# Performance work log

Hardware: AMD Instinct MI355X
Metric: run time of the kernel (lower is better)

The kernel has to match this reference:

```python
import jax, jax.numpy as jnp
import numpy as np

DIM = 1024
N_OBJ = 2048
N_REL = 4096
H_CAT = 4
H_OUT = 6
OUT_CAT = DIM // 2            # 512, concat=True branch
OUT_NC = (DIM // 2) * H_OUT   # 3072, concat=False branch


def setup_inputs() -> dict:
    key = jax.random.key(0)
    ks = jax.random.split(key, 6)
    s = 0.02
    return {
        "feat_obj": jax.random.normal(ks[0], (N_OBJ, DIM), jnp.float32),
        "feat_rel": jax.random.normal(ks[1], (N_REL, DIM), jnp.float32),
        # 3 concat=True attentions, each with 4 Linears(dim -> dim/2)
        "W_cat": jax.random.normal(ks[2], (3, 4, DIM, OUT_CAT), jnp.float32) * s,
        "b_cat": jax.random.normal(ks[3], (3, 4, OUT_CAT), jnp.float32) * s,
        # 2 used concat=False attentions, each with 4 Linears(dim -> 6*dim/2)
        "W_out": jax.random.normal(ks[4], (2, 4, DIM, OUT_NC), jnp.float32) * s,
        "b_out": jax.random.normal(ks[5], (2, 4, OUT_NC), jnp.float32) * s,
    }


def _mha(xq, xk, Ws, bs, h, mask=None, concat=True):
    # Ws: [4, dim, out_dim], bs: [4, out_dim]
    out_dim = Ws.shape[-1]
    d_k = out_dim // h

    def proj(x, W, b):
        return (x @ W + b).reshape(-1, h, d_k).transpose(1, 0, 2)  # [h, N, d_k]

    q = proj(xq, Ws[0], bs[0])
    k = proj(xk, Ws[1], bs[1])
    qv = proj(xq, Ws[2], bs[2])
    kv = proj(xk, Ws[3], bs[3])
    scores = jnp.einsum('hnd,hmd->hnm', q, k) / jnp.sqrt(jnp.asarray(d_k, q.dtype))
    if mask is not None:
        scores = jnp.where(mask == 0, jnp.asarray(-1e9, scores.dtype), scores)
    p = jax.nn.softmax(scores, axis=-1)          # [h, Nq, Nk]
    a1 = jax.nn.elu(jnp.einsum('hnm,hmd->hnd', p, kv))  # per-head value mix (rows)
    a2 = jax.nn.elu(jnp.einsum('hnm,hnd->hmd', p, qv))  # transposed mix (cols)
    if concat:
        nq, nk = xq.shape[0], xk.shape[0]
        return a1.transpose(1, 0, 2).reshape(nq, out_dim), a2.transpose(1, 0, 2).reshape(nk, out_dim)
    return a1.sum(0), a2.sum(0)


def reference(feat_obj, feat_rel, W_cat, b_cat, W_out, b_out):
    n_obj = feat_obj.shape[0]
    mask = 1.0 - jnp.eye(n_obj, dtype=feat_obj.dtype)  # zero out self-attention

    sub_obj, obj_sub = _mha(feat_obj, feat_obj, W_cat[0], b_cat[0], H_CAT, mask, True)
    sub_rel, rel_sub = _mha(feat_obj, feat_rel, W_cat[1], b_cat[1], H_CAT, None, True)
    rel_obj, obj_rel = _mha(feat_rel, feat_obj, W_cat[2], b_cat[2], H_CAT, None, True)

    obj_feat = (feat_obj
                + jnp.concatenate((sub_obj, obj_sub), axis=1)
                + jnp.concatenate((sub_rel, obj_rel), axis=1)) / 3.0
    rel_feat = (feat_rel + jnp.concatenate((rel_obj, rel_sub), axis=1)) / 2.0

    _, rel_sub2 = _mha(obj_feat, rel_feat, W_out[0], b_out[0], H_OUT, None, False)
    rel_obj2, _ = _mha(rel_feat, obj_feat, W_out[1], b_out[1], H_OUT, None, False)
    rel_feat = (feat_rel + jnp.concatenate((rel_obj2, rel_sub2), axis=1)) / 2.0

    return obj_feat, rel_feat
```

## Files before the change

kernel.cpp:

```cpp
#include <hip/hip_runtime.h>

typedef unsigned short u16;
typedef unsigned int u32;
typedef __attribute__((ext_vector_type(4))) float f32x4;
typedef __attribute__((ext_vector_type(8))) __bf16 bf16x8;
typedef __attribute__((ext_vector_type(8))) unsigned short u16x8;

#if defined(__has_builtin)
#if __has_builtin(__builtin_amdgcn_global_load_lds)
#define HAS_GLL 1
#endif
#endif

__device__ __forceinline__ u16 f2bf(float f) {
    u32 u = __builtin_bit_cast(u32, f);
    u += 0x7fffu + ((u >> 16) & 1u);
    return (u16)(u >> 16);
}
__device__ __forceinline__ float bf2f(u16 x) {
    return __builtin_bit_cast(float, (u32)x << 16);
}

template <int N> __device__ __forceinline__ void wbar() {
#ifdef HAS_GLL
    if constexpr (N == 0)
        asm volatile("s_waitcnt vmcnt(0)\n\ts_barrier" ::: "memory");
    else if constexpr (N == 2)
        asm volatile("s_waitcnt vmcnt(2)\n\ts_barrier" ::: "memory");
    else
        asm volatile("s_waitcnt vmcnt(4)\n\ts_barrier" ::: "memory");
#else
    __syncthreads();
#endif
}

__device__ __forceinline__ void fbar() {
#ifdef HAS_GLL
    asm volatile("s_waitcnt vmcnt(0) lgkmcnt(0)\n\ts_barrier" ::: "memory");
#else
    __syncthreads();
#endif
}

__device__ __forceinline__ void lbar() {
#ifdef HAS_GLL
    asm volatile("s_waitcnt lgkmcnt(0)\n\ts_barrier" ::: "memory");
#else
    __syncthreads();
#endif
}

__global__ __launch_bounds__(256) void zero_kernel(float* __restrict__ p, int n) {
    int i = blockIdx.x * 256 + threadIdx.x;
    if (i < n) p[i] = 0.f;
}

__global__ __launch_bounds__(256) void cvt_bf16_kernel(const float4* __restrict__ in,
                                                       ushort4* __restrict__ out, int n4) {
    int i = blockIdx.x * 256 + threadIdx.x;
    if (i < n4) {
        float4 v = in[i];
        ushort4 o;
        o.x = f2bf(v.x); o.y = f2bf(v.y); o.z = f2bf(v.z); o.w = f2bf(v.w);
        out[i] = o;
    }
}

__global__ __launch_bounds__(256) void transcvt_kernel(const float* __restrict__ W,
                                                       u16* __restrict__ Wt, int K, int N) {
    __shared__ u16 t[32][33];
    int b = blockIdx.z;
    const float* Wb = W + (size_t)b * K * N;
    u16* Wtb = Wt + (size_t)b * K * N;
    int n0 = blockIdx.x * 32, k0 = blockIdx.y * 32;
    int tx = threadIdx.x, ty = threadIdx.y;
#pragma unroll
    for (int j = 0; j < 4; ++j)
        t[ty + j * 8][tx] = f2bf(Wb[(size_t)(k0 + ty + j * 8) * N + n0 + tx]);
    __syncthreads();
#pragma unroll
    for (int j = 0; j < 4; ++j)
        Wtb[(size_t)(n0 + ty + j * 8) * K + k0 + tx] = t[tx][ty + j * 8];
}

__global__ __launch_bounds__(256) void scale_rows_kernel(const u16* __restrict__ in,
                                                         u16* __restrict__ out,
                                                         const float* __restrict__ rd,
                                                         int C, int lgdk, int mul) {
    int i = (blockIdx.x * 256 + threadIdx.x) * 8;
    int r = i / C, c = i % C;
    const float* rdp = rd + ((size_t)(r >> lgdk)) * C + c;
    u16x8 x = *reinterpret_cast<const u16x8*>(in + i);
    u16x8 o;
#pragma unroll
    for (int j = 0; j < 8; ++j)
        o[j] = f2bf(mul ? bf2f(x[j]) * rdp[j] : bf2f(x[j]) / rdp[j]);
    *reinterpret_cast<u16x8*>(out + i) = o;
}

struct FGrp { const u16* A; const u16* B; const u16* V; float* O; float* rs; int M; int NK; int mask; };
struct FCfg { FGrp g[3]; };

template <int NORM>
__global__ __launch_bounds__(256) void fused_attn1_kernel(FCfg cfg, float scale) {
    __shared__ __align__(16) u16 Bbuf[2][4 * 2048];
    __shared__ __align__(16) u16 Vbuf[2][2 * 4096];
    __shared__ __align__(16) u16 Pbuf[2 * 2048];
    __shared__ float rsum_lds[64][2];
    const int gi = blockIdx.z >> 2, h = blockIdx.z & 3;
    FGrp G = (gi == 0) ? cfg.g[0] : (gi == 1) ? cfg.g[1] : cfg.g[2];
    const int row0 = blockIdx.x * 64;
    if (row0 >= G.M) return;
    const u16* Ap = G.A + h * 128;
    const u16* Bp = G.B + h * 128;
    const u16* Vp = G.V + (size_t)h * 128 * G.NK;
    float* Op = G.O + h * 128;
    const int ldv = G.NK;
    const int tid = threadIdx.x, lane = tid & 63, wid = tid >> 6;
    const int swr = (wid >> 1) * 32, swc = (wid & 1) * 32;
    const int pwr = swr, pwc = (wid & 1) * 64;

    auto gld = [&](const u16* src, u16* dst) {
#ifdef HAS_GLL
        __builtin_amdgcn_global_load_lds(
            (const __attribute__((address_space(1))) void*)src,
            (__attribute__((address_space(3))) void*)dst, 16, 0, 0);
#else
        *reinterpret_cast<uint4*>(dst) = *reinterpret_cast<const uint4*>(src);
#endif
    };
    auto stageB = [&](int t, int buf) {
#pragma unroll
        for (int it = 0; it < 4; ++it) {
            int c = tid + it * 256;
            int kb = c >> 8, cc = c & 255;
            int r = cc >> 2, lch = (cc & 3) ^ ((r >> 1) & 3);
            gld(Bp + (size_t)(t * 64 + r) * 512 + kb * 32 + lch * 8, &Bbuf[buf][kb * 2048 + cc * 8]);
        }
    };
    auto stageV = [&](int t, int buf) {
#pragma unroll
        for (int it = 0; it < 4; ++it) {
            int c = tid + it * 256;
            int kb = c >> 9, cc = c & 511;
            int r = cc >> 2, lch = (cc & 3) ^ ((r >> 1) & 3);
            gld(Vp + (size_t)r * ldv + t * 64 + kb * 32 + lch * 8, &Vbuf[buf][kb * 4096 + cc * 8]);
        }
    };

    bf16x8 areg[2][4];
#pragma unroll
    for (int m = 0; m < 2; ++m) {
        int rr = swr + m * 16 + (lane & 15);
#pragma unroll
        for (int kk = 0; kk < 4; ++kk)
            areg[m][kk] = *reinterpret_cast<const bf16x8*>(
                Ap + (size_t)(row0 + rr) * 512 + kk * 32 + (lane >> 4) * 8);
    }
    stageB(0, 0);
    stageV(0, 0);
    stageB(1, 1);
    stageV(1, 1);
    fbar();

    f32x4 accp[2][4] = {};
    float rsum[2][4] = {};
    const int nt = G.NK >> 6;
    for (int t = 0; t < nt; ++t) {
        const int cur = t & 1;
        f32x4 accs[2][2] = {};
#pragma unroll
        for (int kk = 0; kk < 4; ++kk) {
            bf16x8 bf[2];
#pragma unroll
            for (int n = 0; n < 2; ++n) {
                int rr = swc + n * 16 + (lane & 15);
                int p = (lane >> 4) ^ ((rr >> 1) & 3);
                bf[n] = *reinterpret_cast<const bf16x8*>(&Bbuf[cur][kk * 2048 + rr * 32 + p * 8]);
            }
#pragma unroll
            for (int m = 0; m < 2; ++m)
#pragma unroll
                for (int n = 0; n < 2; ++n)
                    accs[m][n] = __builtin_amdgcn_mfma_f32_16x16x32_bf16(areg[m][kk], bf[n], accs[m][n], 0, 0, 0);
        }
#pragma unroll
        for (int m = 0; m < 2; ++m) {
#pragma unroll
            for (int n = 0; n < 2; ++n) {
#pragma unroll
                for (int j = 0; j < 4; ++j) {
                    int prow = swr + m * 16 + ((lane >> 4) << 2) + j;
                    int pkey = swc + n * 16 + (lane & 15);
                    float v = __expf(accs[m][n][j] * scale);
                    if (G.mask && (row0 + prow == t * 64 + pkey)) v = 0.f;
                    if (NORM == 1) rsum[m][j] += v;
                    Pbuf[(pkey >> 5) * 2048 + prow * 32 +
                         ((((pkey >> 3) & 3) ^ ((prow >> 1) & 3)) << 3) + (pkey & 7)] = f2bf(v);
                }
            }
        }
        lbar();
        if (t + 2 < nt) stageB(t + 2, cur);
#pragma unroll
        for (int kk = 0; kk < 2; ++kk) {
            bf16x8 pf[2], vf[4];
#pragma unroll
            for (int m = 0; m < 2; ++m) {
                int rr = pwr + m * 16 + (lane & 15);
                int p = (lane >> 4) ^ ((rr >> 1) & 3);
                pf[m] = *reinterpret_cast<const bf16x8*>(&Pbuf[kk * 2048 + rr * 32 + p * 8]);
            }
#pragma unroll
            for (int n = 0; n < 4; ++n) {
                int dd = pwc + n * 16 + (lane & 15);
                int p = (lane >> 4) ^ ((dd >> 1) & 3);
                vf[n] = *reinterpret_cast<const bf16x8*>(&Vbuf[cur][kk * 4096 + dd * 32 + p * 8]);
            }
#pragma unroll
            for (int m = 0; m < 2; ++m)
#pragma unroll
                for (int n = 0; n < 4; ++n)
                    accp[m][n] = __builtin_amdgcn_mfma_f32_16x16x32_bf16(pf[m], vf[n], accp[m][n], 0, 0, 0);
        }
        if (t + 2 < nt)      wbar<4>();
        else if (t + 1 < nt) wbar<0>();
        if (t + 2 < nt) stageV(t + 2, cur);
    }

    if (NORM == 1) {
#pragma unroll
        for (int m = 0; m < 2; ++m)
#pragma unroll
            for (int j = 0; j < 4; ++j) {
                float s = rsum[m][j];
                s += __shfl_xor(s, 1); s += __shfl_xor(s, 2);
                s += __shfl_xor(s, 4); s += __shfl_xor(s, 8);
                rsum[m][j] = s;
            }
        if ((lane & 15) == 0) {
#pragma unroll
            for (int m = 0; m < 2; ++m)
#pragma unroll
                for (int j = 0; j < 4; ++j)
                    rsum_lds[swr + m * 16 + ((lane >> 4) << 2) + j][wid & 1] = rsum[m][j];
        }
        __syncthreads();
        if (tid < 64)
            G.rs[(size_t)h * G.M + row0 + tid] = 1.f / (rsum_lds[tid][0] + rsum_lds[tid][1]);
#pragma unroll
        for (int m = 0; m < 2; ++m) {
#pragma unroll
            for (int j = 0; j < 4; ++j) {
                int row = pwr + m * 16 + ((lane >> 4) << 2) + j;
                float rd = 1.f / (rsum_lds[row][0] + rsum_lds[row][1]);
#pragma unroll
                for (int n = 0; n < 4; ++n) {
                    float v = accp[m][n][j] * rd;
                    v = v > 0.f ? v : (__expf(v) - 1.f);
                    Op[(size_t)(row0 + row) * 512 + pwc + n * 16 + (lane & 15)] = v;
                }
            }
        }
    } else {
#pragma unroll
        for (int m = 0; m < 2; ++m) {
#pragma unroll
            for (int j = 0; j < 4; ++j) {
                int row = pwr + m * 16 + ((lane >> 4) << 2) + j;
#pragma unroll
                for (int n = 0; n < 4; ++n) {
                    float v = accp[m][n][j];
                    v = v > 0.f ? v : (__expf(v) - 1.f);
                    Op[(size_t)(row0 + row) * 512 + pwc + n * 16 + (lane & 15)] = v;
                }
            }
        }
    }
}

enum { E_PROJ = 0, E_PROJT, E_EXP, E_EXPC, E_EXPT, E_EXPMT, E_PART };

template <int EPI, int BM>
__global__ __launch_bounds__(256) void gemm_nt(const u16* __restrict__ A, const u16* __restrict__ B,
                                               void* __restrict__ Cv, void* __restrict__ CvT,
                                               const float* __restrict__ bias, float* __restrict__ rs,
                                               int M, int N, int K, int lda, int ldb, int ldc, int ldcT,
                                               float scale, long sAz, long sBz, long sCz, long sCzT,
                                               long sBias, long sRs, int ZK, long sAz2, long sBz2) {
    constexpr bool HAS_BIAS = (EPI == E_PROJ || EPI == E_PROJT);
    constexpr bool DO_EXP = (EPI == E_EXP || EPI == E_EXPC || EPI == E_EXPT || EPI == E_EXPMT);
    constexpr bool DO_MASK = (EPI == E_EXPMT);
    constexpr int RSUM = (EPI == E_EXPC) ? 2 : (DO_EXP ? 1 : 0);
    constexpr bool STORE_N = (EPI != E_PROJT);
    constexpr bool STORE_T = (EPI == E_PROJT || EPI == E_EXPT || EPI == E_EXPMT);

    constexpr int MF = BM / 32;
    constexpr int ITERS = BM * 32 / (256 * 8);
    constexpr int LOADS = ITERS * 2;
    constexpr int SM_STAGE = 3 * BM * 64;
    constexpr int SM_REPACK = BM * BM;
    __shared__ __align__(16) u16 smem[SM_STAGE > SM_REPACK ? SM_STAGE : SM_REPACK];
    const int tid = threadIdx.x;
    const int lane = tid & 63;
    const int wid = tid >> 6;
    const int wr = (wid >> 1) * (BM / 2);
    const int wc = (wid & 1) * (BM / 2);
    const int row0 = blockIdx.x * BM;
    const int col0 = blockIdx.y * BM;
    const long zo = blockIdx.z;
    const long hz = zo / ZK;
    const long kz = zo - hz * ZK;
    const u16* Az = A + hz * sAz + kz * sAz2;
    const u16* Bz = B + hz * sBz + kz * sBz2;
    const float* biasz = bias ? bias + zo * sBias : nullptr;
    float* rsz = rs ? rs + zo * sRs : nullptr;
    f32x4 acc[MF][MF] = {};

    auto As = [&](int buf) { return smem + buf * (BM * 64); };
    auto Bs = [&](int buf) { return smem + buf * (BM * 64) + BM * 32; };

    auto stage = [&](int buf, int k0) {
#pragma unroll
        for (int i = 0; i < ITERS; ++i) {
            int c = tid + i * 256;
            int r = c >> 2;
            int lch = (c & 3) ^ ((r >> 1) & 3);
            const u16* sa = Az + (size_t)(row0 + r) * lda + k0 + lch * 8;
            const u16* sb = Bz + (size_t)(col0 + r) * ldb + k0 + lch * 8;
#ifdef HAS_GLL
            __builtin_amdgcn_global_load_lds(
                (const __attribute__((address_space(1))) void*)sa,
                (__attribute__((address_space(3))) void*)(&As(buf)[c * 8]), 16, 0, 0);
            __builtin_amdgcn_global_load_lds(
                (const __attribute__((address_space(1))) void*)sb,
                (__attribute__((address_space(3))) void*)(&Bs(buf)[c * 8]), 16, 0, 0);
#else
            *reinterpret_cast<uint4*>(&As(buf)[c * 8]) = *reinterpret_cast<const uint4*>(sa);
            *reinterpret_cast<uint4*>(&Bs(buf)[c * 8]) = *reinterpret_cast<const uint4*>(sb);
#endif
        }
    };

    stage(0, 0);
    stage(1, 32);
    wbar<LOADS>();

    const int nsteps = K >> 5;
    for (int t = 0; t < nsteps; ++t) {
        const int bufc = t % 3;
        const bool more2 = (t + 2 < nsteps);
        if (more2) stage((t + 2) % 3, (t + 2) << 5);
        bf16x8 af[MF], bv[MF];
#pragma unroll
        for (int m = 0; m < MF; ++m) {
            int rr = wr + m * 16 + (lane & 15);
            int p = (lane >> 4) ^ ((rr >> 1) & 3);
            af[m] = *reinterpret_cast<const bf16x8*>(&As(bufc)[rr * 32 + p * 8]);
        }
#pragma unroll
        for (int n = 0; n < MF; ++n) {
            int rr = wc + n * 16 + (lane & 15);
            int p = (lane >> 4) ^ ((rr >> 1) & 3);
            bv[n] = *reinterpret_cast<const bf16x8*>(&Bs(bufc)[rr * 32 + p * 8]);
        }
#pragma unroll
        for (int m = 0; m < MF; ++m)
#pragma unroll
            for (int n = 0; n < MF; ++n)
                acc[m][n] = __builtin_amdgcn_mfma_f32_16x16x32_bf16(af[m], bv[n], acc[m][n], 0, 0, 0);
        if (more2)                 wbar<LOADS>();
        else if (t + 1 < nsteps)   wbar<0>();
        else                       __syncthreads();
    }

#pragma unroll
    for (int m = 0; m < MF; ++m) {
#pragma unroll
        for (int n = 0; n < MF; ++n) {
#pragma unroll
            for (int j = 0; j < 4; ++j) {
                float v = acc[m][n][j];
                if (HAS_BIAS) v += biasz[col0 + wc + n * 16 + (lane & 15)];
                if (DO_EXP) {
                    v = __expf(v * scale);
                    if (DO_MASK &&
                        row0 + wr + m * 16 + ((lane >> 4) << 2) + j ==
                        col0 + wc + n * 16 + (lane & 15)) v = 0.f;
                }
                acc[m][n][j] = v;
            }
        }
    }

    if (RSUM == 1) {
#pragma unroll
        for (int m = 0; m < MF; ++m) {
#pragma unroll
            for (int j = 0; j < 4; ++j) {
                float p = 0.f;
#pragma unroll
                for (int n = 0; n < MF; ++n) p += acc[m][n][j];
                p += __shfl_xor(p, 1); p += __shfl_xor(p, 2);
                p += __shfl_xor(p, 4); p += __shfl_xor(p, 8);
                if ((lane & 15) == 0)
                    atomicAdd(rsz + row0 + wr + m * 16 + ((lane >> 4) << 2) + j, p);
            }
        }
    } else if (RSUM == 2) {
#pragma unroll
        for (int n = 0; n < MF; ++n) {
            float p = 0.f;
#pragma unroll
            for (int m = 0; m < MF; ++m)
#pragma unroll
                for (int j = 0; j < 4; ++j) p += acc[m][n][j];
            p += __shfl_xor(p, 16); p += __shfl_xor(p, 32);
            if (lane < 16) atomicAdd(rsz + col0 + wc + n * 16 + lane, p);
        }
    }

    char* lc = reinterpret_cast<char*>(smem);
    if (STORE_N) {
#pragma unroll
        for (int m = 0; m < MF; ++m) {
#pragma unroll
            for (int n = 0; n < MF; ++n) {
#pragma unroll
                for (int j = 0; j < 4; ++j) {
                    int lrow = wr + m * 16 + ((lane >> 4) << 2) + j;
                    int lcol = wc + n * 16 + (lane & 15);
                    u32 byte = (u32)((lrow * BM + lcol) * 2) ^ (((lrow >> 2) & 3) << 5);
                    *reinterpret_cast<u16*>(lc + byte) = f2bf(acc[m][n][j]);
                }
            }
        }
        __syncthreads();
        constexpr int CH = BM / 8;
        constexpr int NIT = BM * CH / 256;
        u16* Cp = reinterpret_cast<u16*>(Cv) + zo * sCz;
#pragma unroll
        for (int it = 0; it < NIT; ++it) {
            int idx = it * 256 + tid;
            int rrow = idx / CH, c8 = idx % CH;
            u32 byte = (u32)((rrow * BM + c8 * 8) * 2) ^ (((rrow >> 2) & 3) << 5);
            u16x8 val = *reinterpret_cast<const u16x8*>(lc + byte);
            *reinterpret_cast<u16x8*>(Cp + (size_t)(row0 + rrow) * ldc + col0 + c8 * 8) = val;
        }
    }
    if (STORE_T) {
        __syncthreads();
#pragma unroll
        for (int m = 0; m < MF; ++m) {
#pragma unroll
            for (int n = 0; n < MF; ++n) {
                int lcol = wc + n * 16 + (lane & 15);
                int lrow0 = wr + m * 16 + ((lane >> 4) << 2);
                u32 byte = (u32)((lcol * BM + lrow0) * 2) ^ ((u32)(lcol & 7) << 4);
                u32 lo = (u32)f2bf(acc[m][n][0]) | ((u32)f2bf(acc[m][n][1]) << 16);
                u32 hi = (u32)f2bf(acc[m][n][2]) | ((u32)f2bf(acc[m][n][3]) << 16);
                uint2 pk; pk.x = lo; pk.y = hi;
                *reinterpret_cast<uint2*>(lc + byte) = pk;
            }
        }
        __syncthreads();
        constexpr int CHT = BM / 8;
        constexpr int NITT = BM * CHT / 256;
        u16* Tp = reinterpret_cast<u16*>(CvT) + zo * sCzT;
#pragma unroll
        for (int it = 0; it < NITT; ++it) {
            int idx = it * 256 + tid;
            int c = idx / CHT, r8 = idx % CHT;
            u32 byte = (u32)((c * BM + r8 * 8) * 2) ^ ((u32)(c & 7) << 4);
            u16x8 val = *reinterpret_cast<const u16x8*>(lc + byte);
            *reinterpret_cast<u16x8*>(Tp + (size_t)(col0 + c) * ldcT + row0 + r8 * 8) = val;
        }
    }
}

__global__ __launch_bounds__(256) void reduce_h_elu_kernel(const u16* __restrict__ part,
                                                           float* __restrict__ out, int R, int H,
                                                           const float* __restrict__ rd) {
    int i = blockIdx.x * 256 + threadIdx.x;
    int row = i >> 6, c8 = i & 63;
    long plane = (long)R * 512;
    const u16* p = part + (size_t)row * 512 + c8 * 8;
    float s[8] = {};
    for (int h = 0; h < H; ++h) {
        u16x8 x = *reinterpret_cast<const u16x8*>(p + (size_t)h * plane);
        float r = rd ? 1.f / rd[(size_t)h * R + row] : 1.f;
#pragma unroll
        for (int j = 0; j < 8; ++j) {
            float v = bf2f(x[j]) * r;
            s[j] += v > 0.f ? v : (__expf(v) - 1.f);
        }
    }
    float4* o = reinterpret_cast<float4*>(out + (size_t)row * 512 + c8 * 8);
    o[0] = float4{s[0], s[1], s[2], s[3]};
    o[1] = float4{s[4], s[5], s[6], s[7]};
}

__global__ __launch_bounds__(256) void combine_obj_kernel(const float4* __restrict__ feat,
        const float4* __restrict__ a, const float4* __restrict__ b,
        const float4* __restrict__ c, const float4* __restrict__ d,
        float4* __restrict__ out, ushort4* __restrict__ outbf) {
    int i = blockIdx.x * 256 + threadIdx.x;
    int r = i >> 8, c4 = i & 255;
    size_t half = (size_t)r * 128 + (c4 & 127);
    float4 t1 = (c4 < 128) ? a[half] : b[half];
    float4 t2 = (c4 < 128) ? c[half] : d[half];
    float4 f = feat[i];
    float4 o;
    o.x = (f.x + t1.x + t2.x) * (1.f / 3.f);
    o.y = (f.y + t1.y + t2.y) * (1.f / 3.f);
    o.z = (f.z + t1.z + t2.z) * (1.f / 3.f);
    o.w = (f.w + t1.w + t2.w) * (1.f / 3.f);
    out[i] = o;
    ushort4 ob; ob.x = f2bf(o.x); ob.y = f2bf(o.y); ob.z = f2bf(o.z); ob.w = f2bf(o.w);
    outbf[i] = ob;
}

__global__ __launch_bounds__(256) void combine_rel1_kernel(const float4* __restrict__ feat,
        const float4* __restrict__ a, const float4* __restrict__ b, ushort4* __restrict__ outbf) {
    int i = blockIdx.x * 256 + threadIdx.x;
    int r = i >> 8, c4 = i & 255;
    size_t half = (size_t)r * 128 + (c4 & 127);
    float4 t = (c4 < 128) ? a[half] : b[half];
    float4 f = feat[i];
    ushort4 ob;
    ob.x = f2bf((f.x + t.x) * 0.5f); ob.y = f2bf((f.y + t.y) * 0.5f);
    ob.z = f2bf((f.z + t.z) * 0.5f); ob.w = f2bf((f.w + t.w) * 0.5f);
    outbf[i] = ob;
}

__global__ __launch_bounds__(256) void combine_rel2_kernel(const float4* __restrict__ feat,
        const float4* __restrict__ a, const float4* __restrict__ b, float4* __restrict__ out) {
    int i = blockIdx.x * 256 + threadIdx.x;
    int r = i >> 8, c4 = i & 255;
    size_t half = (size_t)r * 128 + (c4 & 127);
    float4 t = (c4 < 128) ? a[half] : b[half];
    float4 f = feat[i];
    float4 o;
    o.x = (f.x + t.x) * 0.5f; o.y = (f.y + t.y) * 0.5f;
    o.z = (f.z + t.z) * 0.5f; o.w = (f.w + t.w) * 0.5f;
    out[i] = o;
}

extern "C" void kernel_launch(void* const* d_in, const int* in_sizes, int n_in,
                              void* d_out, int out_size, void* d_ws, size_t ws_size,
                              hipStream_t stream) {
    (void)in_sizes; (void)n_in; (void)out_size; (void)ws_size;
    const float* feat_obj = (const float*)d_in[0];
    const float* feat_rel = (const float*)d_in[1];
    const float* W_cat = (const float*)d_in[2];
    const float* b_cat = (const float*)d_in[3];
    const float* W_out = (const float*)d_in[4];
    const float* b_out = (const float*)d_in[5];
    float* out_obj = (float*)d_out;
    float* out_rel = (float*)d_out + (size_t)2048 * 1024;

    char* w = (char*)d_ws;
    auto alloc = [&](size_t bytes) { void* p = (void*)w; w += (bytes + 255) & ~(size_t)255; return p; };
    u16* bf_obj  = (u16*)alloc((size_t)2048 * 1024 * 2);
    u16* bf_rel  = (u16*)alloc((size_t)4096 * 1024 * 2);
    u16* bf_obj2 = (u16*)alloc((size_t)2048 * 1024 * 2);
    u16* bf_rel2 = (u16*)alloc((size_t)4096 * 1024 * 2);
    u16* Wt_cat  = (u16*)alloc((size_t)12 * 512 * 1024 * 2);
    u16* Q01   = (u16*)alloc((size_t)2 * 2048 * 512 * 2);
    u16* K02   = (u16*)alloc((size_t)2 * 2048 * 512 * 2);
    u16* Q2    = (u16*)alloc((size_t)4096 * 512 * 2);
    u16* K1    = (u16*)alloc((size_t)4096 * 512 * 2);
    u16* Vq01T = (u16*)alloc((size_t)2 * 512 * 2048 * 2);
    u16* Vk02T = (u16*)alloc((size_t)2 * 512 * 2048 * 2);
    u16* Vk1T  = (u16*)alloc((size_t)512 * 4096 * 2);
    u16* Vq2T  = (u16*)alloc((size_t)512 * 4096 * 2);
    u16* Pq2   = (u16*)alloc((size_t)2 * 2048 * 3072 * 2);
    u16* Pk2   = (u16*)alloc((size_t)2 * 4096 * 3072 * 2);
    u16* VTa   = (u16*)alloc((size_t)2 * 3072 * 2048 * 2);
    u16* VTs   = (u16*)alloc((size_t)3072 * 2048 * 2);
    u16* Sbuf  = (u16*)alloc((size_t)6 * 4096 * 2048 * 2);
    u16* Wt2   = Sbuf;
    u16* part  = (u16*)alloc((size_t)6 * 4096 * 512 * 2);
    float* rdAll = (float*)alloc((size_t)36864 * 4);
    float* rdQ = rdAll;
    float* rdM = rdAll + 12288;
    float* rs0 = (float*)alloc((size_t)4 * 2048 * 4);
    float* rs1 = (float*)alloc((size_t)4 * 2048 * 4);
    float* rs2 = (float*)alloc((size_t)4 * 4096 * 4);
    float* sub_obj  = (float*)alloc((size_t)2048 * 512 * 4);
    float* obj_sub  = (float*)alloc((size_t)2048 * 512 * 4);
    float* sub_rel  = (float*)alloc((size_t)2048 * 512 * 4);
    float* obj_rel  = (float*)alloc((size_t)2048 * 512 * 4);
    float* rel_obj  = (float*)alloc((size_t)4096 * 512 * 4);
    float* rel_sub  = (float*)alloc((size_t)4096 * 512 * 4);
    float* rel_obj2 = (float*)alloc((size_t)4096 * 512 * 4);
    float* rel_sub2 = (float*)alloc((size_t)4096 * 512 * 4);

    zero_kernel<<<144, 256, 0, stream>>>(rdAll, 36864);
    cvt_bf16_kernel<<<2048, 256, 0, stream>>>((const float4*)feat_obj, (ushort4*)bf_obj, 2048 * 1024 / 4);
    cvt_bf16_kernel<<<4096, 256, 0, stream>>>((const float4*)feat_rel, (ushort4*)bf_rel, 4096 * 1024 / 4);
    transcvt_kernel<<<dim3(16, 32, 12), dim3(32, 8), 0, stream>>>(W_cat, Wt_cat, 1024, 512);
    transcvt_kernel<<<dim3(96, 32, 8), dim3(32, 8), 0, stream>>>(W_out, Wt2, 1024, 3072);

    const float sc1 = 0.08838834764831845f;
    const float sc2 = 0.04419417382415922f;
    const long planeW = (long)512 * 1024;
    const long planeW2 = (long)3072 * 1024;
    const long NIL = 0;

    gemm_nt<E_PROJ, 64><<<dim3(32, 8, 2), 256, 0, stream>>>(
        bf_obj, Wt_cat, Q01, nullptr, b_cat, nullptr,
        2048, 512, 1024, 1024, 1024, 512, 0, 0.f, NIL, 4 * planeW, (long)2048 * 512, NIL,
        4L * 512, NIL, 1, NIL, NIL);
    gemm_nt<E_PROJ, 64><<<dim3(32, 8, 2), 256, 0, stream>>>(
        bf_obj, Wt_cat + planeW, K02, nullptr, b_cat + 512, nullptr,
        2048, 512, 1024, 1024, 1024, 512, 0, 0.f, NIL, 8 * planeW, (long)2048 * 512, NIL,
        8L * 512, NIL, 1, NIL, NIL);
    gemm_nt<E_PROJT, 64><<<dim3(32, 8, 2), 256, 0, stream>>>(
        bf_obj, Wt_cat + 2 * planeW, nullptr, Vq01T, b_cat + 1024, nullptr,
        2048, 512, 1024, 1024, 1024, 0, 2048, 0.f, NIL, 4 * planeW, NIL, (long)512 * 2048,
        4L * 512, NIL, 1, NIL, NIL);
    gemm_nt<E_PROJT, 64><<<dim3(32, 8, 2), 256, 0, stream>>>(
        bf_obj, Wt_cat + 3 * planeW, nullptr, Vk02T, b_cat + 1536, nullptr,
        2048, 512, 1024, 1024, 1024, 0, 2048, 0.f, NIL, 8 * planeW, NIL, (long)512 * 2048,
        8L * 512, NIL, 1, NIL, NIL);
    gemm_nt<E_PROJ, 64><<<dim3(64, 8, 1), 256, 0, stream>>>(
        bf_rel, Wt_cat + 5 * planeW, K1, nullptr, b_cat + 5 * 512, nullptr,
        4096, 512, 1024, 1024, 1024, 512, 0, 0.f, NIL, NIL, NIL, NIL, NIL, NIL, 1, NIL, NIL);
    gemm_nt<E_PROJ, 64><<<dim3(64, 8, 1), 256, 0, stream>>>(
        bf_rel, Wt_cat + 8 * planeW, Q2, nullptr, b_cat + 8 * 512, nullptr,
        4096, 512, 1024, 1024, 1024, 512, 0, 0.f, NIL, NIL, NIL, NIL, NIL, NIL, 1, NIL, NIL);
    gemm_nt<E_PROJT, 64><<<dim3(64, 8, 1), 256, 0, stream>>>(
        bf_rel, Wt_cat + 7 * planeW, nullptr, Vk1T, b_cat + 7 * 512, nullptr,
        4096, 512, 1024, 1024, 1024, 0, 4096, 0.f, NIL, NIL, NIL, NIL, NIL, NIL, 1, NIL, NIL);
    gemm_nt<E_PROJT, 64><<<dim3(64, 8, 1), 256, 0, stream>>>(
        bf_rel, Wt_cat + 10 * planeW, nullptr, Vq2T, b_cat + 10 * 512, nullptr,
        4096, 512, 1024, 1024, 1024, 0, 4096, 0.f, NIL, NIL, NIL, NIL, NIL, NIL, 1, NIL, NIL);

    FCfg f1, f2;
    f1.g[0] = { Q01,                    K02,                    Vk02T,                    sub_obj, rs0, 2048, 2048, 1 };
    f1.g[1] = { Q01 + (size_t)2048*512, K1,                     Vk1T,                     sub_rel, rs1, 2048, 4096, 0 };
    f1.g[2] = { Q2,                     K02 + (size_t)2048*512, Vk02T + (size_t)512*2048, rel_obj, rs2, 4096, 2048, 0 };
    fused_attn1_kernel<1><<<dim3(64, 1, 12), 256, 0, stream>>>(f1, sc1);
    scale_rows_kernel<<<512, 256, 0, stream>>>(Vq01T, Vq01T, rs0, 2048, 7, 1);
    scale_rows_kernel<<<512, 256, 0, stream>>>(Vq01T + (size_t)512 * 2048, Vq01T + (size_t)512 * 2048, rs1, 2048, 7, 1);
    scale_rows_kernel<<<1024, 256, 0, stream>>>(Vq2T, Vq2T, rs2, 4096, 7, 1);
    f2.g[0] = { K02,                    Q01,                    Vq01T,                    obj_sub, rs0, 2048, 2048, 1 };
    f2.g[1] = { K1,                     Q01 + (size_t)2048*512, Vq01T + (size_t)512*2048, rel_sub, rs1, 4096, 2048, 0 };
    f2.g[2] = { K02 + (size_t)2048*512, Q2,                     Vq2T,                     obj_rel, rs2, 2048, 4096, 0 };
    fused_attn1_kernel<0><<<dim3(64, 1, 12), 256, 0, stream>>>(f2, sc1);

    combine_obj_kernel<<<2048, 256, 0, stream>>>((const float4*)feat_obj, (const float4*)sub_obj,
        (const float4*)obj_sub, (const float4*)sub_rel, (const float4*)obj_rel,
        (float4*)out_obj, (ushort4*)bf_obj2);
    combine_rel1_kernel<<<4096, 256, 0, stream>>>((const float4*)feat_rel, (const float4*)rel_obj,
        (const float4*)rel_sub, (ushort4*)bf_rel2);

    gemm_nt<E_PROJ, 128><<<dim3(16, 24, 2), 256, 0, stream>>>(
        bf_obj2, Wt2, Pq2, nullptr, b_out, nullptr,
        2048, 3072, 1024, 1024, 1024, 3072, 0, 0.f, NIL, 5 * planeW2, (long)2048 * 3072, NIL,
        5L * 3072, NIL, 1, NIL, NIL);
    gemm_nt<E_PROJ, 128><<<dim3(32, 24, 2), 256, 0, stream>>>(
        bf_rel2, Wt2 + planeW2, Pk2, nullptr, b_out + 3072, nullptr,
        4096, 3072, 1024, 1024, 1024, 3072, 0, 0.f, NIL, 3 * planeW2, (long)4096 * 3072, NIL,
        3L * 3072, NIL, 1, NIL, NIL);
    gemm_nt<E_PROJT, 128><<<dim3(16, 24, 2), 256, 0, stream>>>(
        bf_obj2, Wt2 + 2 * planeW2, nullptr, VTa, b_out + 2 * 3072, nullptr,
        2048, 3072, 1024, 1024, 1024, 0, 2048, 0.f, NIL, 5 * planeW2, NIL, (long)3072 * 2048,
        5L * 3072, NIL, 1, NIL, NIL);

    const long spl2 = (long)4096 * 2048;
    const long vpl2 = (long)4096 * 512;

    {
        gemm_nt<E_EXPC, 128><<<dim3(32, 16, 6), 256, 0, stream>>>(
            Pk2, Pq2, Sbuf, nullptr, nullptr, rdQ,
            4096, 2048, 512, 3072, 3072, 2048, 0, sc2, 512, 512, spl2, NIL, NIL, 2048, 1, NIL, NIL);
        scale_rows_kernel<<<3072, 256, 0, stream>>>(VTa, VTs, rdQ, 2048, 9, 0);
        gemm_nt<E_PART, 128><<<dim3(32, 4, 6), 256, 0, stream>>>(
            Sbuf, VTs, part, nullptr, nullptr, nullptr,
            4096, 512, 2048, 2048, 2048, 512, 0, 0.f, spl2, 512L * 2048, vpl2, NIL, NIL, NIL,
            1, NIL, NIL);
        reduce_h_elu_kernel<<<1024, 256, 0, stream>>>(part, rel_sub2, 4096, 6, nullptr);
    }
    {
        gemm_nt<E_EXP, 128><<<dim3(32, 16, 6), 256, 0, stream>>>(
            Pk2 + (size_t)4096 * 3072, Pq2 + (size_t)2048 * 3072, Sbuf, nullptr, nullptr, rdM,
            4096, 2048, 512, 3072, 3072, 2048, 0, sc2, 512, 512, spl2, NIL, NIL, 4096, 1, NIL, NIL);
        gemm_nt<E_PART, 128><<<dim3(32, 4, 6), 256, 0, stream>>>(
            Sbuf, VTa + (size_t)3072 * 2048, part, nullptr, nullptr, nullptr,
            4096, 512, 2048, 2048, 2048, 512, 0, 0.f, spl2, 512L * 2048, vpl2, NIL, NIL, NIL,
            1, NIL, NIL);
        reduce_h_elu_kernel<<<1024, 256, 0, stream>>>(part, rel_obj2, 4096, 6, rdM);
    }

    combine_rel2_kernel<<<4096, 256, 0, stream>>>((const float4*)feat_rel, (const float4*)rel_obj2,
        (const float4*)rel_sub2, (float4*)out_rel);
}
```

Measured before the change: 818.1 us.

## Permute concat-branch weights to batch stage-one projections into four GEMM launches

Reorders the twelve concat-branch weight matrices and their biases at conversion time so that projections sharing an input and output layout sit contiguously. The eight stage-one projection GEMMs become four batched launches, and their tile size moves from 64 to 128. Downstream attention groups and scaling kernels are repointed to the new consolidated buffers. This cuts launch overhead and small-grid underutilisation, at the cost of an extra bias permutation kernel and fewer, larger tiles per launch.

New measurement: 792.9 us (median of 2 runs). 1.03x faster.

```diff
diff --git a/kernel.cpp b/kernel.cpp
--- a/kernel.cpp
+++ b/kernel.cpp
@@ -50,6 +50,14 @@
 #endif
 }
 
+__device__ __forceinline__ int s1perm(int b) {
+    switch (b) {
+        case 0: return 0;  case 1: return 2;  case 2: return 4;  case 3: return 6;
+        case 4: return 1;  case 5: return 8;  case 6: return 5;  case 7: return 10;
+        case 8: return 9;  case 9: return 3;  case 10: return 11; default: return 7;
+    }
+}
+
 __global__ __launch_bounds__(256) void zero_kernel(float* __restrict__ p, int n) {
     int i = blockIdx.x * 256 + threadIdx.x;
     if (i < n) p[i] = 0.f;
@@ -81,6 +89,32 @@
 #pragma unroll
     for (int j = 0; j < 4; ++j)
         Wtb[(size_t)(n0 + ty + j * 8) * K + k0 + tx] = t[tx][ty + j * 8];
+}
+
+__global__ __launch_bounds__(256) void transcvt_perm_kernel(const float* __restrict__ W,
+                                                            u16* __restrict__ Wt, int K, int N) {
+    __shared__ u16 t[32][33];
+    int b = blockIdx.z;
+    int d = s1perm(b);
+    const float* Wb = W + (size_t)b * K * N;
+    u16* Wtb = Wt + (size_t)d * K * N;
+    int n0 = blockIdx.x * 32, k0 = blockIdx.y * 32;
+    int tx = threadIdx.x, ty = threadIdx.y;
+#pragma unroll
+    for (int j = 0; j < 4; ++j)
+        t[ty + j * 8][tx] = f2bf(Wb[(size_t)(k0 + ty + j * 8) * N + n0 + tx]);
+    __syncthreads();
+#pragma unroll
+    for (int j = 0; j < 4; ++j)
+        Wtb[(size_t)(n0 + ty + j * 8) * K + k0 + tx] = t[tx][ty + j * 8];
+}
+
+__global__ __launch_bounds__(256) void bias_perm_kernel(const float* __restrict__ in,
+                                                        float* __restrict__ out) {
+    int b = blockIdx.x;
+    int d = s1perm(b);
+    out[d * 512 + threadIdx.x] = in[b * 512 + threadIdx.x];
+    out[d * 512 + 256 + threadIdx.x] = in[b * 512 + 256 + threadIdx.x];
 }
 
 __global__ __launch_bounds__(256) void scale_rows_kernel(const u16* __restrict__ in,
@@ -565,15 +599,12 @@
     u16* bf_rel  = (u16*)alloc((size_t)4096 * 1024 * 2);
     u16* bf_obj2 = (u16*)alloc((size_t)2048 * 1024 * 2);
     u16* bf_rel2 = (u16*)alloc((size_t)4096 * 1024 * 2);
-    u16* Wt_cat  = (u16*)alloc((size_t)12 * 512 * 1024 * 2);
-    u16* Q01   = (u16*)alloc((size_t)2 * 2048 * 512 * 2);
-    u16* K02   = (u16*)alloc((size_t)2 * 2048 * 512 * 2);
-    u16* Q2    = (u16*)alloc((size_t)4096 * 512 * 2);
-    u16* K1    = (u16*)alloc((size_t)4096 * 512 * 2);
-    u16* Vq01T = (u16*)alloc((size_t)2 * 512 * 2048 * 2);
-    u16* Vk02T = (u16*)alloc((size_t)2 * 512 * 2048 * 2);
-    u16* Vk1T  = (u16*)alloc((size_t)512 * 4096 * 2);
-    u16* Vq2T  = (u16*)alloc((size_t)512 * 4096 * 2);
+    u16* WtP     = (u16*)alloc((size_t)12 * 512 * 1024 * 2);
+    float* rbcat = (float*)alloc((size_t)12 * 512 * 4);
+    u16* QKo   = (u16*)alloc((size_t)4 * 2048 * 512 * 2);
+    u16* RelN  = (u16*)alloc((size_t)2 * 4096 * 512 * 2);
+    u16* To    = (u16*)alloc((size_t)4 * 512 * 2048 * 2);
+    u16* RelT  = (u16*)alloc((size_t)2 * 512 * 4096 * 2);
     u16* Pq2   = (u16*)alloc((size_t)2 * 2048 * 3072 * 2);
     u16* Pk2   = (u16*)alloc((size_t)2 * 4096 * 3072 * 2);
     u16* VTa   = (u16*)alloc((size_t)2 * 3072 * 2048 * 2);
@@ -599,7 +630,8 @@
     zero_kernel<<<144, 256, 0, stream>>>(rdAll, 36864);
     cvt_bf16_kernel<<<2048, 256, 0, stream>>>((const float4*)feat_obj, (ushort4*)bf_obj, 2048 * 1024 / 4);
     cvt_bf16_kernel<<<4096, 256, 0, stream>>>((const float4*)feat_rel, (ushort4*)bf_rel, 4096 * 1024 / 4);
-    transcvt_kernel<<<dim3(16, 32, 12), dim3(32, 8), 0, stream>>>(W_cat, Wt_cat, 1024, 512);
+    transcvt_perm_kernel<<<dim3(16, 32, 12), dim3(32, 8), 0, stream>>>(W_cat, WtP, 1024, 512);
+    bias_perm_kernel<<<12, 256, 0, stream>>>(b_cat, rbcat);
     transcvt_kernel<<<dim3(96, 32, 8), dim3(32, 8), 0, stream>>>(W_out, Wt2, 1024, 3072);
 
     const float sc1 = 0.08838834764831845f;
@@ -607,47 +639,35 @@
     const long planeW = (long)512 * 1024;
     const long planeW2 = (long)3072 * 1024;
     const long NIL = 0;
-
-    gemm_nt<E_PROJ, 64><<<dim3(32, 8, 2), 256, 0, stream>>>(
-        bf_obj, Wt_cat, Q01, nullptr, b_cat, nullptr,
-        2048, 512, 1024, 1024, 1024, 512, 0, 0.f, NIL, 4 * planeW, (long)2048 * 512, NIL,
-        4L * 512, NIL, 1, NIL, NIL);
-    gemm_nt<E_PROJ, 64><<<dim3(32, 8, 2), 256, 0, stream>>>(
-        bf_obj, Wt_cat + planeW, K02, nullptr, b_cat + 512, nullptr,
-        2048, 512, 1024, 1024, 1024, 512, 0, 0.f, NIL, 8 * planeW, (long)2048 * 512, NIL,
-        8L * 512, NIL, 1, NIL, NIL);
-    gemm_nt<E_PROJT, 64><<<dim3(32, 8, 2), 256, 0, stream>>>(
-        bf_obj, Wt_cat + 2 * planeW, nullptr, Vq01T, b_cat + 1024, nullptr,
-        2048, 512, 1024, 1024, 1024, 0, 2048, 0.f, NIL, 4 * planeW, NIL, (long)512 * 2048,
-        4L * 512, NIL, 1, NIL, NIL);
-    gemm_nt<E_PROJT, 64><<<dim3(32, 8, 2), 256, 0, stream>>>(
-        bf_obj, Wt_cat + 3 * planeW, nullptr, Vk02T, b_cat + 1536, nullptr,
-        2048, 512, 1024, 1024, 1024, 0, 2048, 0.f, NIL, 8 * planeW, NIL, (long)512 * 2048,
-        8L * 512, NIL, 1, NIL, NIL);
-    gemm_nt<E_PROJ, 64><<<dim3(64, 8, 1), 256, 0, stream>>>(
-        bf_rel, Wt_cat + 5 * planeW, K1, nullptr, b_cat + 5 * 512, nullptr,
-        4096, 512, 1024, 1024, 1024, 512, 0, 0.f, NIL, NIL, NIL, NIL, NIL, NIL, 1, NIL, NIL);
-    gemm_nt<E_PROJ, 64><<<dim3(64, 8, 1), 256, 0, stream>>>(
-        bf_rel, Wt_cat + 8 * planeW, Q2, nullptr, b_cat + 8 * 512, nullptr,
-        4096, 512, 1024, 1024, 1024, 512, 0, 0.f, NIL, NIL, NIL, NIL, NIL, NIL, 1, NIL, NIL);
-    gemm_nt<E_PROJT, 64><<<dim3(64, 8, 1), 256, 0, stream>>>(
-        bf_rel, Wt_cat + 7 * planeW, nullptr, Vk1T, b_cat + 7 * 512, nullptr,
-        4096, 512, 1024, 1024, 1024, 0, 4096, 0.f, NIL, NIL, NIL, NIL, NIL, NIL, 1, NIL, NIL);
-    gemm_nt<E_PROJT, 64><<<dim3(64, 8, 1), 256, 0, stream>>>(
-        bf_rel, Wt_cat + 10 * planeW, nullptr, Vq2T, b_cat + 10 * 512, nullptr,
-        4096, 512, 1024, 1024, 1024, 0, 4096, 0.f, NIL, NIL, NIL, NIL, NIL, NIL, 1, NIL, NIL);
+    const long pQ = (long)2048 * 512;
+    const long pRN = (long)4096 * 512;
+    const long pT = (long)512 * 2048;
+    const long pRT = (long)512 * 4096;
+
+    gemm_nt<E_PROJ, 128><<<dim3(16, 4, 4), 256, 0, stream>>>(
+        bf_obj, WtP, QKo, nullptr, rbcat, nullptr,
+        2048, 512, 1024, 1024, 1024, 512, 0, 0.f, NIL, planeW, pQ, NIL, 512, NIL, 1, NIL, NIL);
+    gemm_nt<E_PROJT, 128><<<dim3(16, 4, 4), 256, 0, stream>>>(
+        bf_obj, WtP + 4 * planeW, nullptr, To, rbcat + 4 * 512, nullptr,
+        2048, 512, 1024, 1024, 1024, 0, 2048, 0.f, NIL, planeW, NIL, pT, 512, NIL, 1, NIL, NIL);
+    gemm_nt<E_PROJ, 128><<<dim3(32, 4, 2), 256, 0, stream>>>(
+        bf_rel, WtP + 8 * planeW, RelN, nullptr, rbcat + 8 * 512, nullptr,
+        4096, 512, 1024, 1024, 1024, 512, 0, 0.f, NIL, planeW, pRN, NIL, 512, NIL, 1, NIL, NIL);
+    gemm_nt<E_PROJT, 128><<<dim3(32, 4, 2), 256, 0, stream>>>(
+        bf_rel, WtP + 10 * planeW, nullptr, RelT, rbcat + 10 * 512, nullptr,
+        4096, 512, 1024, 1024, 1024, 0, 4096, 0.f, NIL, planeW, NIL, pRT, 512, NIL, 1, NIL, NIL);
 
     FCfg f1, f2;
-    f1.g[0] = { Q01,                    K02,                    Vk02T,                    sub_obj, rs0, 2048, 2048, 1 };
-    f1.g[1] = { Q01 + (size_t)2048*512, K1,                     Vk1T,                     sub_rel, rs1, 2048, 4096, 0 };
-    f1.g[2] = { Q2,                     K02 + (size_t)2048*512, Vk02T + (size_t)512*2048, rel_obj, rs2, 4096, 2048, 0 };
+    f1.g[0] = { QKo,          QKo + 2 * pQ, To + 2 * pT,  sub_obj, rs0, 2048, 2048, 1 };
+    f1.g[1] = { QKo + pQ,     RelN,         RelT,         sub_rel, rs1, 2048, 4096, 0 };
+    f1.g[2] = { RelN + pRN,   QKo + 3 * pQ, To + 3 * pT,  rel_obj, rs2, 4096, 2048, 0 };
     fused_attn1_kernel<1><<<dim3(64, 1, 12), 256, 0, stream>>>(f1, sc1);
-    scale_rows_kernel<<<512, 256, 0, stream>>>(Vq01T, Vq01T, rs0, 2048, 7, 1);
-    scale_rows_kernel<<<512, 256, 0, stream>>>(Vq01T + (size_t)512 * 2048, Vq01T + (size_t)512 * 2048, rs1, 2048, 7, 1);
-    scale_rows_kernel<<<1024, 256, 0, stream>>>(Vq2T, Vq2T, rs2, 4096, 7, 1);
-    f2.g[0] = { K02,                    Q01,                    Vq01T,                    obj_sub, rs0, 2048, 2048, 1 };
-    f2.g[1] = { K1,                     Q01 + (size_t)2048*512, Vq01T + (size_t)512*2048, rel_sub, rs1, 4096, 2048, 0 };
-    f2.g[2] = { K02 + (size_t)2048*512, Q2,                     Vq2T,                     obj_rel, rs2, 2048, 4096, 0 };
+    scale_rows_kernel<<<512, 256, 0, stream>>>(To, To, rs0, 2048, 7, 1);
+    scale_rows_kernel<<<512, 256, 0, stream>>>(To + pT, To + pT, rs1, 2048, 7, 1);
+    scale_rows_kernel<<<1024, 256, 0, stream>>>(RelT + pRT, RelT + pRT, rs2, 4096, 7, 1);
+    f2.g[0] = { QKo + 2 * pQ, QKo,          To,           obj_sub, rs0, 2048, 2048, 1 };
+    f2.g[1] = { RelN,         QKo + pQ,     To + pT,      rel_sub, rs1, 4096, 2048, 0 };
+    f2.g[2] = { QKo + 3 * pQ, RelN + pRN,   RelT + pRT,   obj_rel, rs2, 2048, 4096, 0 };
     fused_attn1_kernel<0><<<dim3(64, 1, 12), 256, 0, stream>>>(f2, sc1);
 
     combine_obj_kernel<<<2048, 256, 0, stream>>>((const float4*)feat_obj, (const float4*)sub_obj,
```
